# Performance work log

Hardware: AMD Instinct MI355X
Metric: run time of the kernel (lower is better)

Reference implementation:

```python
import jax, jax.numpy as jnp
import numpy as np

N = 4096       # nodes
E = 131072     # edges (avg degree 32)
IN_C = 512
HID = 512
OUT_C = 64
RANK = 64      # svd_q
N_DOM = 4
EPS = 1e-5     # BatchNorm eps


def setup_inputs() -> dict:
    key = jax.random.key(0)
    ks = jax.random.split(key, 12)
    x = jax.random.normal(ks[0], (N, IN_C), dtype=jnp.float32)
    row = jax.random.randint(ks[1], (E,), 0, N)
    off = jax.random.randint(ks[2], (E,), 1, N)
    col = (row + off) % N  # guarantee no pre-existing self loops
    edge_index = jnp.stack([row, col]).astype(jnp.int32)
    edge_weight = jax.random.uniform(ks[3], (E,), dtype=jnp.float32)
    y = jax.random.randint(ks[4], (N,), 0, N_DOM).astype(jnp.int32)
    W1 = jax.random.normal(ks[5], (IN_C, HID), dtype=jnp.float32) / np.sqrt(IN_C).astype(np.float32)
    b1 = jnp.zeros((HID,), jnp.float32)
    Wmu = jax.random.normal(ks[6], (HID, OUT_C), dtype=jnp.float32) / np.sqrt(HID).astype(np.float32)
    bmu = jnp.zeros((OUT_C,), jnp.float32)
    Wlv = jax.random.normal(ks[7], (HID, OUT_C), dtype=jnp.float32) / np.sqrt(HID).astype(np.float32)
    blv = jnp.zeros((OUT_C,), jnp.float32)
    gamma = jnp.ones((N_DOM, HID), jnp.float32)   # per-domain BN weight
    beta = jnp.zeros((N_DOM, HID), jnp.float32)   # per-domain BN bias
    return dict(x=x, edge_index=edge_index, edge_weight=edge_weight, y=y,
                W1=W1, b1=b1, Wmu=Wmu, bmu=bmu, Wlv=Wlv, blv=blv,
                gamma=gamma, beta=beta)


def _safe_rsqrt(deg):
    # PyG gcn_norm: deg^-0.5 with inf (and here non-positive) masked to 0
    safe = jnp.where(deg > 0, deg, 1.0)
    return jnp.where(deg > 0, 1.0 / jnp.sqrt(safe), 0.0)


def gcn_conv_edges(x, W, b, row, col, w, n):
    # GCNConv with edge weights: add remaining self loops (fill=1), symmetric norm
    loop = jnp.arange(n, dtype=row.dtype)
    row_f = jnp.concatenate([row, loop])
    col_f = jnp.concatenate([col, loop])
    w_f = jnp.concatenate([w, jnp.ones((n,), w.dtype)])
    deg = jax.ops.segment_sum(w_f, col_f, num_segments=n)
    dinv = _safe_rsqrt(deg)
    norm = dinv[row_f] * w_f * dinv[col_f]
    xw = x @ W                                   # [n, out]
    out = jax.ops.segment_sum(norm[:, None] * xw[row_f], col_f, num_segments=n)
    return out + b


def gcn_conv_dense(x, W, b, A):
    # Dense-adjacency GCNConv (reconstructed adjacency already has a diagonal,
    # so add_remaining_self_loops is a no-op). deg over target (col) index.
    deg = A.sum(axis=0)
    dinv = _safe_rsqrt(deg)
    Ahat = dinv[:, None] * A * dinv[None, :]     # [n, n] normalized
    return Ahat.T @ (x @ W) + b                  # aggregate at targets


def svd_lowrank_recon(A, q, niter=2):
    # torch.svd_lowrank-style randomized SVD, then U @ diag(s) @ V^T
    omega = jax.random.normal(jax.random.key(42), (A.shape[1], q), A.dtype)
    Qb = jnp.linalg.qr(A @ omega)[0]
    for _ in range(niter):
        Qb = jnp.linalg.qr(A.T @ Qb)[0]
        Qb = jnp.linalg.qr(A @ Qb)[0]
    B = Qb.T @ A                                 # [q, n]
    U, s, Vt = jnp.linalg.svd(B, full_matrices=False)
    return (Qb @ (U * s)) @ Vt                   # [n, n] low-rank reconstruction


def dsbn_relu(x, y, gamma, beta):
    # Domain-specific BatchNorm (training-mode batch stats per domain) + ReLU
    out = jnp.zeros_like(x)
    for i in range(N_DOM):
        m = (y == i)
        mf = m.astype(x.dtype)[:, None]
        cnt = jnp.maximum(mf.sum(), 1.0)
        mean = (x * mf).sum(0) / cnt
        var = (((x - mean) ** 2) * mf).sum(0) / cnt   # biased var, as BatchNorm
        xn = (x - mean) / jnp.sqrt(var + EPS) * gamma[i] + beta[i]
        out = jnp.where(m[:, None], xn, out)
    return jax.nn.relu(out)


def reference(x, edge_index, edge_weight, y, W1, b1, Wmu, bmu, Wlv, blv, gamma, beta):
    row, col = edge_index[0], edge_index[1]
    # ----- branch 1: original sparse graph -----
    h1 = dsbn_relu(gcn_conv_edges(x, W1, b1, row, col, edge_weight, N), y, gamma, beta)
    z_mean1 = gcn_conv_edges(h1, Wmu, bmu, row, col, edge_weight, N)
    z_log1 = gcn_conv_edges(h1, Wlv, blv, row, col, edge_weight, N)
    # ----- branch 2: SVD low-rank reconstructed (dense) graph -----
    A = jnp.zeros((N, N), x.dtype).at[row, col].add(edge_weight)  # coalesced COO
    A2 = svd_lowrank_recon(A, RANK)
    h2 = dsbn_relu(gcn_conv_dense(x, W1, b1, A2), y, gamma, beta)
    z_mean2 = gcn_conv_dense(h2, Wmu, bmu, A2)
    z_log2 = gcn_conv_dense(h2, Wlv, blv, A2)
    return (z_mean1, z_log1, z_mean2, z_log2)
```

## Files before the change

### kernel.cpp

```cpp
#include <hip/hip_runtime.h>
#include <hip/hip_bf16.h>


#define NN    4096
#define NEDG  131072
#define INC   512
#define HIDC  512
#define OUTC  64
#define RK    64
#define NDOM  4
#define EPSBN 1e-5f

typedef unsigned short ushortT;
typedef __attribute__((ext_vector_type(8))) short bf16x8;
typedef __attribute__((ext_vector_type(4))) float f32x4;

static inline int cdiv(int a, int b){ return (a + b - 1) / b; }

__device__ __forceinline__ float bf2f(unsigned u){ return __uint_as_float(u << 16); }

__global__ __launch_bounds__(256) void k_detect(const unsigned short* __restrict__ p,
                                                int* __restrict__ flag){
  int t = threadIdx.x;
  int cnt = 0;
  for (int i = t; i < 4096; i += 256){
    unsigned short v = p[2*i];
    int e = (v >> 7) & 0xFF;
    if (e >= 100 && e <= 140) cnt++;
  }
  __shared__ int sh[256];
  sh[t] = cnt; __syncthreads();
  for (int off = 128; off > 0; off >>= 1){ if (t < off) sh[t] += sh[t+off]; __syncthreads(); }
  if (t == 0) *flag = (sh[0] >= 2048) ? 0 : 1;
}

__device__ __forceinline__ float upc1(const void* s, int f, int off){
  return f ? ((const float*)s)[off]
           : __bfloat162float(((const __hip_bfloat16*)s)[off]);
}
__device__ __forceinline__ ushortT tobf(float v){
  __hip_bfloat16 h = __float2bfloat16(v);
  return *(ushortT*)&h;
}
#define SEG_X   2097152
#define SEG_W1  262144
#define SEG_W   131072
#define SEG_WMU 32768
#define SEG_GB  2048
#define SEG_B1  512
#define SEG_BO  64
#define OFF1 (SEG_X)
#define OFF2 (OFF1+SEG_W1)
#define OFF3 (OFF2+SEG_W)
#define OFF4 (OFF3+SEG_WMU)
#define OFF5 (OFF4+SEG_WMU)
#define OFF6 (OFF5+SEG_GB)
#define OFF7 (OFF6+SEG_GB)
#define OFF8 (OFF7+SEG_B1)
#define OFF9 (OFF8+SEG_BO)
#define OFFT (OFF9+SEG_BO)

__global__ __launch_bounds__(256) void k_upcast_all(
    const void* x, const void* W1, const void* w, const void* Wmu, const void* Wlv,
    const void* gm, const void* bt, const void* b1, const void* bmu, const void* blv,
    const int* __restrict__ isf32,
    float* dx, float* dW1, float* dw, float* dWmu, float* dWlv,
    float* dgm, float* dbt, float* db1, float* dbmu, float* dblv,
    ushortT* xbf, ushortT* W1bf, ushortT* Wmubf, ushortT* Wlvbf){
  int i = blockIdx.x*256 + threadIdx.x;
  if (i >= OFFT) return;
  int f = *isf32;
  if      (i < OFF1){ float v = upc1(x, f, i); dx[i] = v; xbf[i] = tobf(v); }
  else if (i < OFF2){ float v = upc1(W1, f, i - OFF1); dW1[i - OFF1] = v; W1bf[i - OFF1] = tobf(v); }
  else if (i < OFF3) dw  [i - OFF2] = upc1(w,   f, i - OFF2);
  else if (i < OFF4){ float v = upc1(Wmu, f, i - OFF3); dWmu[i - OFF3] = v; Wmubf[i - OFF3] = tobf(v); }
  else if (i < OFF5){ float v = upc1(Wlv, f, i - OFF4); dWlv[i - OFF4] = v; Wlvbf[i - OFF4] = tobf(v); }
  else if (i < OFF6) dgm [i - OFF5] = upc1(gm,  f, i - OFF5);
  else if (i < OFF7) dbt [i - OFF6] = upc1(bt,  f, i - OFF6);
  else if (i < OFF8) db1 [i - OFF7] = upc1(b1,  f, i - OFF7);
  else if (i < OFF9) dbmu[i - OFF8] = upc1(bmu, f, i - OFF8);
  else               dblv[i - OFF9] = upc1(blv, f, i - OFF9);
}

__global__ __launch_bounds__(256) void k_prep(float* deg, int* cntR, int* cntC, int* dcnt,
                                              float* bnsum){
  int i = blockIdx.x*256 + threadIdx.x;
  if (i < NN){ deg[i] = 1.0f; cntR[i] = 0; cntC[i] = 0; }
  if (i < NDOM) dcnt[i] = 0;
  if (i < 8*HIDC) bnsum[i] = 0.f;
}
__global__ __launch_bounds__(256) void k_fin(const double* __restrict__ Qd,
        float* __restrict__ Bf1, const double* __restrict__ Cd, float* __restrict__ Cm,
        const double* __restrict__ qs, float* __restrict__ dinv2,
        float* __restrict__ Tm, float* __restrict__ Um, float* __restrict__ bnsum){
  int i = blockIdx.x*256 + threadIdx.x;
  if (i < NN*RK){ Bf1[i] = (float)Qd[i]; Cm[i] = (float)Cd[i]; }
  if (i < NN){
    double s = 0.0;
    #pragma unroll
    for (int k = 0; k < RK; k++) s += Cd[(size_t)i*RK + k] * qs[k];
    dinv2[i] = (s > 0.0) ? (float)(1.0/sqrt(s)) : 0.f;
  }
  if (i < RK*HIDC) Tm[i] = 0.f;
  if (i < 2*RK*RK) Um[i] = 0.f;
  if (i < 8*HIDC)  bnsum[i] = 0.f;
}

__global__ __launch_bounds__(256) void k_hist(const int* __restrict__ row, const int* __restrict__ col,
                                              const float* __restrict__ w, float* deg,
                                              int* cntR, int* cntC){
  int e = blockIdx.x*256 + threadIdx.x;
  if (e < NEDG){
    atomicAdd(&deg[col[e]], w[e]);
    atomicAdd(&cntR[row[e]], 1);
    atomicAdd(&cntC[col[e]], 1);
  }
}
__global__ __launch_bounds__(256) void k_dinv(const float* deg, float* dinv, int n){
  int i = blockIdx.x*256 + threadIdx.x;
  if (i < n){ float d = deg[i]; dinv[i] = (d > 0.f) ? 1.f/sqrtf(d) : 0.f; }
}
__global__ __launch_bounds__(256) void k_norm1(const int* __restrict__ row, const int* __restrict__ col,
                                               const float* __restrict__ w, const float* __restrict__ dinv,
                                               float* __restrict__ nrm){
  int e = blockIdx.x*256 + threadIdx.x;
  if (e < NEDG) nrm[e] = dinv[row[e]] * w[e] * dinv[col[e]];
}
__global__ __launch_bounds__(1024) void k_scan4096(const int* __restrict__ cnt,
                                                   int* __restrict__ ptr, int* __restrict__ pos){
  __shared__ int sh[1024];
  int t = threadIdx.x;
  int b = t*4;
  int a0 = cnt[b], a1 = cnt[b+1], a2 = cnt[b+2], a3 = cnt[b+3];
  sh[t] = a0 + a1 + a2 + a3;
  __syncthreads();
  for (int off = 1; off < 1024; off <<= 1){
    int v = (t >= off) ? sh[t-off] : 0;
    __syncthreads();
    sh[t] += v;
    __syncthreads();
  }
  int excl = (t == 0) ? 0 : sh[t-1];
  ptr[b]   = excl;            pos[b]   = excl;
  ptr[b+1] = excl+a0;         pos[b+1] = excl+a0;
  ptr[b+2] = excl+a0+a1;      pos[b+2] = excl+a0+a1;
  ptr[b+3] = excl+a0+a1+a2;   pos[b+3] = excl+a0+a1+a2;
  if (t == 1023) ptr[4096] = sh[1023];
}
__global__ __launch_bounds__(256) void k_scatter(const int* __restrict__ row, const int* __restrict__ col,
                                                 int* posR, int* posC, int* eidR, int* eidC){
  int e = blockIdx.x*256 + threadIdx.x;
  if (e < NEDG){
    int p = atomicAdd(&posR[row[e]], 1); eidR[p] = e;
    int q = atomicAdd(&posC[col[e]], 1); eidC[q] = e;
  }
}
__global__ __launch_bounds__(256) void k_edges(const int* __restrict__ rowA, const int* __restrict__ colA,
        const float* __restrict__ wf, const float* __restrict__ nrm,
        const int* __restrict__ eidR, const int* __restrict__ eidC,
        int* __restrict__ csrSrc, float* __restrict__ csrW,
        int* __restrict__ cscSrc, float* __restrict__ cscW, float* __restrict__ cscN){
  int p = blockIdx.x*256 + threadIdx.x;
  if (p < NEDG){
    int eR = eidR[p]; csrSrc[p] = colA[eR]; csrW[p] = wf[eR];
    int eC = eidC[p]; cscSrc[p] = rowA[eC]; cscW[p] = wf[eC]; cscN[p] = nrm[eC];
  }
}
__global__ __launch_bounds__(256) void k_dcnt(const int* __restrict__ y, int* dcnt){
  int i = blockIdx.x*256 + threadIdx.x;
  if (i < NN) atomicAdd(&dcnt[y[i]], 1);
}

__device__ __forceinline__ unsigned rotl32(unsigned x, unsigned d){ return (x << d) | (x >> (32u - d)); }
#define TF_ROUND4(R0,R1,R2,R3) \
  x0 += x1; x1 = rotl32(x1,R0); x1 ^= x0; \
  x0 += x1; x1 = rotl32(x1,R1); x1 ^= x0; \
  x0 += x1; x1 = rotl32(x1,R2); x1 ^= x0; \
  x0 += x1; x1 = rotl32(x1,R3); x1 ^= x0;

__device__ __forceinline__ void tf2x32(unsigned k0, unsigned k1, unsigned c0, unsigned c1,
                                       unsigned* o0, unsigned* o1){
  unsigned ks2 = 0x1BD11BDAu ^ k0 ^ k1;
  unsigned x0 = c0 + k0, x1 = c1 + k1;
  TF_ROUND4(13,15,26,6);   x0 += k1;  x1 += ks2 + 1u;
  TF_ROUND4(17,29,16,24);  x0 += ks2; x1 += k0 + 2u;
  TF_ROUND4(13,15,26,6);   x0 += k0;  x1 += k1 + 3u;
  TF_ROUND4(17,29,16,24);  x0 += k1;  x1 += ks2 + 4u;
  TF_ROUND4(13,15,26,6);   x0 += ks2; x1 += k0 + 5u;
  *o0 = x0; *o1 = x1;
}

__device__ double erfinv64(double x){
  double w = -log1p(-x*x);
  double p;
  if (w < 5.0){
    w -= 2.5;
    p = 2.81022636e-08;  p = p*w + 3.43273939e-07; p = p*w - 3.5233877e-06;
    p = p*w - 4.39150654e-06; p = p*w + 0.00021858087; p = p*w - 0.00125372503;
    p = p*w - 0.00417768164;  p = p*w + 0.246640727;   p = p*w + 1.50140941;
  } else {
    w = sqrt(w) - 3.0;
    p = -0.000200214257; p = p*w + 0.000100950558; p = p*w + 0.00134934322;
    p = p*w - 0.00367342844; p = p*w + 0.00573950773; p = p*w - 0.0076224613;
    p = p*w + 0.00943887047; p = p*w + 1.00167406;    p = p*w + 2.83297682;
  }
  double y = p * x;
  const double c = 1.1283791670955126;
  #pragma unroll
  for (int it = 0; it < 3; it++){
    double err = erf(y) - x;
    y -= err / (c * exp(-y*y));
  }
  return y;
}

__device__ float bits_to_normal(unsigned b){
  float f = __uint_as_float((b >> 9) | 0x3f800000u) - 1.0f;
  const float lo = -0.99999994f;
  float x = fmaxf(lo, f * 2.0f + lo);
  double r = 1.4142135623730951 * erfinv64((double)x);
  return (float)r;
}

__global__ __launch_bounds__(256) void k_omega(float* __restrict__ om, double* __restrict__ Gd){
  int i = blockIdx.x*256 + threadIdx.x;
  if (i < RK*RK) Gd[i] = 0.0;
  if (i >= 262144) return;
  unsigned o0, o1;
  tf2x32(0u, 42u, 0u, (unsigned)i, &o0, &o1);
  om[i] = bits_to_normal(o0 ^ o1);
}

__global__ __launch_bounds__(256) void k_gemm_bf16(
    const ushortT* __restrict__ A, const ushortT* __restrict__ B,
    float* __restrict__ Cc, ushortT* __restrict__ Cbf){
  __shared__ ushortT As2[64][40];
  __shared__ ushortT Bs2[64][40];
  int t = threadIdx.x;
  int bm = blockIdx.y * 64, bn = blockIdx.x * 64;
  int w = t >> 6, l = t & 63;
  int lr = l & 15, lk = l >> 4;
  f32x4 acc[4] = {};
  int ar = t >> 2, ac = (t & 3) * 8;
  int bc = t & 63, bk = (t >> 6) * 8;
  for (int k0 = 0; k0 < 512; k0 += 32){
    *(uint4*)&As2[ar][ac] = *(const uint4*)&A[(size_t)(bm + ar) * 512 + k0 + ac];
    ushortT tmp[8];
    #pragma unroll
    for (int j = 0; j < 8; j++)
      tmp[j] = B[(size_t)(k0 + bk + j) * 512 + bn + bc];
    *(uint4*)&Bs2[bc][bk] = *(uint4*)tmp;
    __syncthreads();
    bf16x8 afrag = *(bf16x8*)&As2[w * 16 + lr][lk * 8];
    #pragma unroll
    for (int nt = 0; nt < 4; nt++){
      bf16x8 bfrag = *(bf16x8*)&Bs2[nt * 16 + lr][lk * 8];
      acc[nt] = __builtin_amdgcn_mfma_f32_16x16x32_bf16(afrag, bfrag, acc[nt], 0, 0, 0);
    }
    __syncthreads();
  }
  #pragma unroll
  for (int nt = 0; nt < 4; nt++){
    #pragma unroll
    for (int i = 0; i < 4; i++){
      size_t idx = (size_t)(bm + w * 16 + lk * 4 + i) * 512 + bn + nt * 16 + lr;
      float v = acc[nt][i];
      Cc[idx] = v;
      Cbf[idx] = tobf(v);
    }
  }
}

__device__ __forceinline__ void d_hw2(int bx, int t,
    const ushortT* __restrict__ A, const ushortT* __restrict__ Bm,
    const ushortT* __restrict__ Bl, float* __restrict__ Ca, float* __restrict__ Cb){
  __shared__ ushortT As2[64][40];
  __shared__ ushortT Bs2[64][40];
  int nb = NN/64;
  int second = bx >= nb;
  int bm = (bx - (second ? nb : 0)) * 64;
  const ushortT* B = second ? Bl : Bm;
  float* Cc = second ? Cb : Ca;
  int w = t >> 6, l = t & 63;
  int lr = l & 15, lk = l >> 4;
  f32x4 acc[4] = {};
  int ar = t >> 2, ac = (t & 3) * 8;
  int bc = t & 63, bk = (t >> 6) * 8;
  for (int k0 = 0; k0 < 512; k0 += 32){
    *(uint4*)&As2[ar][ac] = *(const uint4*)&A[(size_t)(bm + ar) * 512 + k0 + ac];
    ushortT tmp[8];
    #pragma unroll
    for (int j = 0; j < 8; j++)
      tmp[j] = B[(size_t)(k0 + bk + j) * 64 + bc];
    *(uint4*)&Bs2[bc][bk] = *(uint4*)tmp;
    __syncthreads();
    bf16x8 afrag = *(bf16x8*)&As2[w * 16 + lr][lk * 8];
    #pragma unroll
    for (int nt = 0; nt < 4; nt++){
      bf16x8 bfrag = *(bf16x8*)&Bs2[nt * 16 + lr][lk * 8];
      acc[nt] = __builtin_amdgcn_mfma_f32_16x16x32_bf16(afrag, bfrag, acc[nt], 0, 0, 0);
    }
    __syncthreads();
  }
  #pragma unroll
  for (int nt = 0; nt < 4; nt++){
    #pragma unroll
    for (int i = 0; i < 4; i++){
      Cc[(size_t)(bm + w * 16 + lk * 4 + i) * 64 + nt * 16 + lr] = acc[nt][i];
    }
  }
}
__global__ __launch_bounds__(256) void k_gemm_hw2(
    const ushortT* __restrict__ A, const ushortT* __restrict__ Bm,
    const ushortT* __restrict__ Bl, float* __restrict__ Ca, float* __restrict__ Cb){
  d_hw2(blockIdx.x, threadIdx.x, A, Bm, Bl, Ca, Cb);
}

__global__ __launch_bounds__(256) void k_gemm_nn(int M, int Nn, int K,
      const float* __restrict__ A, int lda, const float* __restrict__ B, int ldb,
      float* __restrict__ Cc, int ldc, const float* __restrict__ rowscale,
      const float* __restrict__ kscale, const float* __restrict__ bias){
  __shared__ float As[16][65];
  __shared__ float Bs[16][65];
  int bm = blockIdx.y*64, bn = blockIdx.x*64;
  int t = threadIdx.x;
  int tr = t >> 4, tc = t & 15;
  float acc[4][4] = {};
  for (int k0 = 0; k0 < K; k0 += 16){
    #pragma unroll
    for (int q = 0; q < 4; q++){
      int idx = t*4 + q;
      int m = idx >> 4, kk = idx & 15;
      As[kk][m] = A[(size_t)(bm+m)*lda + (k0+kk)];
    }
    #pragma unroll
    for (int q = 0; q < 4; q++){
      int idx = t + q*256;
      int kk = idx >> 6, n = idx & 63;
      float ks = kscale ? kscale[k0+kk] : 1.0f;
      Bs[kk][n] = B[(size_t)(k0+kk)*ldb + (bn+n)] * ks;
    }
    __syncthreads();
    #pragma unroll
    for (int kk = 0; kk < 16; kk++){
      float a0 = As[kk][tr*4+0], a1 = As[kk][tr*4+1], a2 = As[kk][tr*4+2], a3 = As[kk][tr*4+3];
      float b0 = Bs[kk][tc*4+0], b1 = Bs[kk][tc*4+1], b2 = Bs[kk][tc*4+2], b3 = Bs[kk][tc*4+3];
      acc[0][0] += a0*b0; acc[0][1] += a0*b1; acc[0][2] += a0*b2; acc[0][3] += a0*b3;
      acc[1][0] += a1*b0; acc[1][1] += a1*b1; acc[1][2] += a1*b2; acc[1][3] += a1*b3;
      acc[2][0] += a2*b0; acc[2][1] += a2*b1; acc[2][2] += a2*b2; acc[2][3] += a2*b3;
      acc[3][0] += a3*b0; acc[3][1] += a3*b1; acc[3][2] += a3*b2; acc[3][3] += a3*b3;
    }
    __syncthreads();
  }
  #pragma unroll
  for (int i2 = 0; i2 < 4; i2++){
    int m = bm + tr*4 + i2;
    float rs = rowscale ? rowscale[m] : 1.0f;
    #pragma unroll
    for (int j2 = 0; j2 < 4; j2++){
      int n = bn + tc*4 + j2;
      float v = acc[i2][j2] * rs;
      if (bias) v += bias[n];
      Cc[(size_t)m*ldc + n] = v;
    }
  }
}

__global__ __launch_bounds__(256) void k_gemm_nn2(
      const float* __restrict__ A, const float* __restrict__ Um,
      const float* __restrict__ rowscale,
      const float* __restrict__ bmu, const float* __restrict__ blv,
      float* __restrict__ zout){
  __shared__ float As[16][65];
  __shared__ float Bs[16][65];
  int z = blockIdx.z;
  const float* B = Um + (size_t)z*RK*RK;
  const float* bias = z ? blv : bmu;
  float* Cc = zout + (size_t)(2+z)*NN*OUTC;
  int bm = blockIdx.y*64;
  int t = threadIdx.x;
  int tr = t >> 4, tc = t & 15;
  float acc[4][4] = {};
  for (int k0 = 0; k0 < RK; k0 += 16){
    #pragma unroll
    for (int q = 0; q < 4; q++){
      int idx = t*4 + q;
      int m = idx >> 4, kk = idx & 15;
      As[kk][m] = A[(size_t)(bm+m)*RK + (k0+kk)];
    }
    #pragma unroll
    for (int q = 0; q < 4; q++){
      int idx = t + q*256;
      int kk = idx >> 6, n = idx & 63;
      Bs[kk][n] = B[(size_t)(k0+kk)*RK + n];
    }
    __syncthreads();
    #pragma unroll
    for (int kk = 0; kk < 16; kk++){
      float a0 = As[kk][tr*4+0], a1 = As[kk][tr*4+1], a2 = As[kk][tr*4+2], a3 = As[kk][tr*4+3];
      float b0 = Bs[kk][tc*4+0], b1 = Bs[kk][tc*4+1], b2 = Bs[kk][tc*4+2], b3 = Bs[kk][tc*4+3];
      acc[0][0] += a0*b0; acc[0][1] += a0*b1; acc[0][2] += a0*b2; acc[0][3] += a0*b3;
      acc[1][0] += a1*b0; acc[1][1] += a1*b1; acc[1][2] += a1*b2; acc[1][3] += a1*b3;
      acc[2][0] += a2*b0; acc[2][1] += a2*b1; acc[2][2] += a2*b2; acc[2][3] += a2*b3;
      acc[3][0] += a3*b0; acc[3][1] += a3*b1; acc[3][2] += a3*b2; acc[3][3] += a3*b3;
    }
    __syncthreads();
  }
  #pragma unroll
  for (int i2 = 0; i2 < 4; i2++){
    int m = bm + tr*4 + i2;
    float rs = rowscale[m];
    #pragma unroll
    for (int j2 = 0; j2 < 4; j2++){
      int n = tc*4 + j2;
      Cc[(size_t)m*OUTC + n] = acc[i2][j2] * rs + bias[n];
    }
  }
}

__global__ __launch_bounds__(256) void k_gemm_tn_sk(int M, int Nn, int K, int kchunk,
      const float* __restrict__ A, int lda, const float* __restrict__ B, int ldb,
      float* __restrict__ Cc, int ldc, const float* __restrict__ kscale){
  __shared__ float As[32][17];
  __shared__ float Bs[32][17];
  int bm = blockIdx.y*16, bn = blockIdx.x*16;
  int kb = blockIdx.z*kchunk, ke = kb + kchunk;
  int t = threadIdx.x;
  int tm = t >> 4, tn = t & 15;
  float acc = 0.f;
  for (int k0 = kb; k0 < ke; k0 += 32){
    #pragma unroll
    for (int q = 0; q < 2; q++){
      int idx = t + q*256;
      int kk = idx >> 4, m = idx & 15;
      float sv = kscale ? kscale[k0+kk] : 1.0f;
      As[kk][m] = A[(size_t)(k0+kk)*lda + (bm+m)] * sv;
      Bs[kk][m] = B[(size_t)(k0+kk)*ldb + (bn+m)];
    }
    __syncthreads();
    #pragma unroll
    for (int kk = 0; kk < 32; kk++) acc += As[kk][tm] * Bs[kk][tn];
    __syncthreads();
  }
  atomicAdd(&Cc[(size_t)(bm+tm)*ldc + (bn+tn)], acc);
}

__global__ __launch_bounds__(256) void k_gemm_tn_sk2(
      const float* __restrict__ A,
      const float* __restrict__ Ba, const float* __restrict__ Bb,
      float* __restrict__ Um, const float* __restrict__ kscale){
  __shared__ float As[32][17];
  __shared__ float Bs[32][17];
  int z = blockIdx.z;
  int second = z >= 16;
  int kb = (second ? z - 16 : z) * 256, ke = kb + 256;
  const float* B = second ? Bb : Ba;
  float* Cc = Um + (second ? RK*RK : 0);
  int bm = blockIdx.y*16, bn = blockIdx.x*16;
  int t = threadIdx.x;
  int tm = t >> 4, tn = t & 15;
  float acc = 0.f;
  for (int k0 = kb; k0 < ke; k0 += 32){
    #pragma unroll
    for (int q = 0; q < 2; q++){
      int idx = t + q*256;
      int kk = idx >> 4, m = idx & 15;
      As[kk][m] = A[(size_t)(k0+kk)*RK + (bm+m)] * kscale[k0+kk];
      Bs[kk][m] = B[(size_t)(k0+kk)*OUTC + (bn+m)];
    }
    __syncthreads();
    #pragma unroll
    for (int kk = 0; kk < 32; kk++) acc += As[kk][tm] * Bs[kk][tn];
    __syncthreads();
  }
  atomicAdd(&Cc[(size_t)(bm+tm)*RK + (bn+tn)], acc);
}

__global__ __launch_bounds__(64) void k_spmm32(const int* __restrict__ ptr,
                       const int* __restrict__ src, const float* __restrict__ cf,
                       const float* __restrict__ X, float* __restrict__ Y){
  int seg = blockIdx.x;
  int t = threadIdx.x;
  double acc = 0.0;
  int p0 = ptr[seg], p1 = ptr[seg+1];
  for (int p = p0; p < p1; ++p){
    acc += (double)cf[p] * (double)X[(size_t)src[p]*RK + t];
  }
  Y[(size_t)seg*RK + t] = (float)acc;
}
__global__ __launch_bounds__(64) void k_spmm32to64(const int* __restrict__ ptr,
                       const int* __restrict__ src, const float* __restrict__ cf,
                       const float* __restrict__ X, double* __restrict__ Y){
  int seg = blockIdx.x;
  int t = threadIdx.x;
  double acc = 0.0;
  int p0 = ptr[seg], p1 = ptr[seg+1];
  for (int p = p0; p < p1; ++p){
    acc += (double)cf[p] * (double)X[(size_t)src[p]*RK + t];
  }
  Y[(size_t)seg*RK + t] = acc;
}
__global__ __launch_bounds__(256) void k_gram64(const double* __restrict__ X, double* __restrict__ G){
  __shared__ double Xs[64][65];
  int b = blockIdx.x;
  int t = threadIdx.x;
  #pragma unroll
  for (int q = 0; q < 16; q++){
    int idx = t + q*256;
    Xs[idx >> 6][idx & 63] = X[(size_t)(b*64 + (idx >> 6))*RK + (idx & 63)];
  }
  __syncthreads();
  int i = t >> 2;
  int j0 = (t & 3) * 16;
  double acc[16];
  #pragma unroll
  for (int jj = 0; jj < 16; jj++) acc[jj] = 0.0;
  for (int k = 0; k < 64; k++){
    double a = Xs[k][i];
    #pragma unroll
    for (int jj = 0; jj < 16; jj++) acc[jj] += a * Xs[k][j0+jj];
  }
  #pragma unroll
  for (int jj = 0; jj < 16; jj++) atomicAdd(&G[i*RK + j0 + jj], acc[jj]);
}

#define CHOLF_CHUNK(I0) \
  for (int k2 = 0; k2 < 16; k2++){ \
    int k = (I0) + k2; \
    int buf = k & 1; \
    if (t < 64 && j == k){ \
      double d = sqrt(fmax(cdiag, 1e-300)); \
      double s = 1.0 / d; \
      myd = d; \
      sdd[k] = s; \
      _Pragma("unroll") \
      for (int i = (I0); i < 64; i++){ c[i] *= s; colk[buf][i] = c[i]; } \
    } \
    __syncthreads(); \
    if (t < 64 && j > k && j < 64){ \
      double cj = colk[buf][j]; \
      cdiag -= cj * cj; \
      _Pragma("unroll") \
      for (int i = (I0); i < 64; i++){ c[i] -= colk[buf][i] * cj; } \
    } \
    __syncthreads(); \
  }

__global__ __launch_bounds__(256) void k_chol_spmm(
    double* __restrict__ G, double* __restrict__ sdd,
    const int* __restrict__ ptr, const int* __restrict__ src, const float* __restrict__ cf,
    const ushortT* __restrict__ Xb, float* __restrict__ Y,
    const float* __restrict__ self_dinv, const float* __restrict__ bias){
  __shared__ double colk[2][64];
  int t = threadIdx.x;
  if (blockIdx.x == 0){
    int j = t;
    double c[64];
    double cdiag = 0.0, myd = 0.0;
    if (t < 64){
      #pragma unroll
      for (int i = 0; i < 64; i++) c[i] = G[i*64 + j];
      #pragma unroll
      for (int i = 0; i < 64; i++) if (i == j) cdiag = c[i];
    }
    CHOLF_CHUNK(0)
    CHOLF_CHUNK(16)
    CHOLF_CHUNK(32)
    CHOLF_CHUNK(48)
    if (t < 64){
      #pragma unroll
      for (int i = 0; i < 64; i++){
        double v = (i > j) ? c[i] : 0.0;
        if (i == j) v = myd;
        G[i*64 + j] = v;
      }
    }
  } else {
    int seg = blockIdx.x - 1;
    float acc0, acc1;
    {
      float sd = self_dinv[seg]; float s2 = sd*sd;
      unsigned v = *(const unsigned*)&Xb[(size_t)seg*HIDC + 2*t];
      acc0 = s2 * bf2f(v & 0xffffu);
      acc1 = s2 * bf2f(v >> 16);
    }
    int p0 = ptr[seg], p1 = ptr[seg+1];
    for (int p = p0; p < p1; ++p){
      int o = src[p];
      float cc = cf[p];
      unsigned v = *(const unsigned*)&Xb[(size_t)o*HIDC + 2*t];
      acc0 += cc * bf2f(v & 0xffffu);
      acc1 += cc * bf2f(v >> 16);
    }
    acc0 += bias[2*t];
    acc1 += bias[2*t+1];
    Y[(size_t)seg*HIDC + 2*t]     = acc0;
    Y[(size_t)seg*HIDC + 2*t + 1] = acc1;
  }
}

__device__ __forceinline__ void d_bnpart(int b, int t,
    const float* __restrict__ H, const int* __restrict__ y, float* __restrict__ bnsum){
  int j0 = 2*t;
  float s00=0,s01=0,s10=0,s11=0,s20=0,s21=0,s30=0,s31=0;
  float q00=0,q01=0,q10=0,q11=0,q20=0,q21=0,q30=0,q31=0;
  int r0 = b*32;
  for (int r = r0; r < r0+32; r++){
    int d = y[r];
    float2 v = *(const float2*)&H[(size_t)r*HIDC + j0];
    float ax = v.x, ay = v.y;
    float bx = ax*ax, by = ay*ay;
    if      (d == 0){ s00+=ax; s01+=ay; q00+=bx; q01+=by; }
    else if (d == 1){ s10+=ax; s11+=ay; q10+=bx; q11+=by; }
    else if (d == 2){ s20+=ax; s21+=ay; q20+=bx; q21+=by; }
    else            { s30+=ax; s31+=ay; q30+=bx; q31+=by; }
  }
  atomicAdd(&bnsum[0*HIDC+j0], s00); atomicAdd(&bnsum[0*HIDC+j0+1], s01);
  atomicAdd(&bnsum[1*HIDC+j0], s10); atomicAdd(&bnsum[1*HIDC+j0+1], s11);
  atomicAdd(&bnsum[2*HIDC+j0], s20); atomicAdd(&bnsum[2*HIDC+j0+1], s21);
  atomicAdd(&bnsum[3*HIDC+j0], s30); atomicAdd(&bnsum[3*HIDC+j0+1], s31);
  atomicAdd(&bnsum[4*HIDC+j0], q00); atomicAdd(&bnsum[4*HIDC+j0+1], q01);
  atomicAdd(&bnsum[5*HIDC+j0], q10); atomicAdd(&bnsum[5*HIDC+j0+1], q11);
  atomicAdd(&bnsum[6*HIDC+j0], q20); atomicAdd(&bnsum[6*HIDC+j0+1], q21);
  atomicAdd(&bnsum[7*HIDC+j0], q30); atomicAdd(&bnsum[7*HIDC+j0+1], q31);
}
__global__ __launch_bounds__(256) void k_bnpart(const float* __restrict__ H,
        const int* __restrict__ y, float* __restrict__ bnsum){
  d_bnpart(blockIdx.x, threadIdx.x, H, y, bnsum);
}

__device__ __forceinline__ void d_bnapply(int idx,
    float* __restrict__ H, const int* __restrict__ y,
    const float* __restrict__ bnsum, const int* __restrict__ dcnt,
    const float* __restrict__ gamma, const float* __restrict__ beta,
    ushortT* __restrict__ Hbf){
  int n = idx >> 9, j = idx & (HIDC-1);
  int d = y[n];
  float cnt  = fmaxf((float)dcnt[d], 1.0f);
  float mean = bnsum[d*HIDC + j] / cnt;
  float var  = fmaxf(bnsum[(4+d)*HIDC + j] / cnt - mean*mean, 0.f);
  float inv  = 1.0f / sqrtf(var + EPSBN);
  float gmm  = gamma[d*HIDC + j];
  float scal = gmm * inv;
  float shft = beta[d*HIDC + j] - mean * gmm * inv;
  float v = H[idx] * scal + shft;
  v = v > 0.f ? v : 0.f;
  H[idx] = v;
  Hbf[idx] = tobf(v);
}
__global__ __launch_bounds__(256) void k_bnapply(float* __restrict__ H, const int* __restrict__ y,
        const float* __restrict__ bnsum, const int* __restrict__ dcnt,
        const float* __restrict__ gamma, const float* __restrict__ beta,
        ushortT* __restrict__ Hbf){
  int idx = blockIdx.x*256 + threadIdx.x;
  if (idx < NN*HIDC) d_bnapply(idx, H, y, bnsum, dcnt, gamma, beta, Hbf);
}

__global__ __launch_bounds__(256) void k_trinv_bn(const double* __restrict__ L,
      const double* __restrict__ sdd, double* __restrict__ Rinv,
      const float* __restrict__ H, const int* __restrict__ y, float* __restrict__ bnsum){
  int t = threadIdx.x;
  if (blockIdx.x > 0){
    d_bnpart(blockIdx.x - 1, t, H, y, bnsum);
    return;
  }
  __shared__ double gl[64][65];
  __shared__ double Xl[64][65];
  __shared__ double sdinv[64];
  __shared__ double Sl[3][16][17];
  #pragma unroll
  for (int q = 0; q < 16; q++){
    int idx = t + (q << 8);
    gl[idx >> 6][idx & 63] = L[idx];
  }
  if (t < 64) sdinv[t] = sdd[t];
  for (int idx = t; idx < 64*65; idx += 256)
    ((double*)Xl)[idx] = 0.0;
  __syncthreads();
  if (t < 64){
    int b = t >> 4, c2 = t & 15;
    int g0 = b << 4;
    int gc = g0 + c2;
    Xl[gc][gc] = sdinv[gc];
    for (int i = c2 - 1; i >= 0; i--){
      int gi = g0 + i;
      double s = 0.0;
      for (int k2 = i + 1; k2 <= c2; k2++)
        s += gl[g0 + k2][gi] * Xl[g0 + k2][gc];
      Xl[gi][gc] = -s * sdinv[gi];
    }
  }
  __syncthreads();
  for (int d = 1; d < 4; d++){
    int np = 4 - d;
    int tot = np << 8;
    for (int e = t; e < tot; e += 256){
      int p = e >> 8;
      int i = (e >> 4) & 15, jj = e & 15;
      int gi = (p << 4) + i, gj = ((p + d) << 4) + jj;
      double s = 0.0;
      int a0 = (p + 1) << 4, a1 = (p + d + 1) << 4;
      for (int a = a0; a < a1; a++)
        s += gl[a][gi] * Xl[a][gj];
      Sl[p][i][jj] = s;
    }
    __syncthreads();
    for (int e = t; e < tot; e += 256){
      int p = e >> 8;
      int i = (e >> 4) & 15, jj = e & 15;
      int gi = (p << 4) + i, gj = ((p + d) << 4) + jj;
      double s = 0.0;
      #pragma unroll
      for (int k2 = 0; k2 < 16; k2++)
        s += Xl[gi][(p << 4) + k2] * Sl[p][k2][jj];
      Xl[gi][gj] = -s;
    }
    __syncthreads();
  }
  #pragma unroll
  for (int q = 0; q < 16; q++){
    int e2 = t + (q << 8);
    Rinv[e2] = Xl[e2 >> 6][e2 & 63];
  }
}

__global__ __launch_bounds__(256) void k_applyR_bn(const double* __restrict__ srcQ,
      const double* __restrict__ Rinv, double* __restrict__ dst,
      float* __restrict__ H, const int* __restrict__ y,
      const float* __restrict__ bnsum, const int* __restrict__ dcnt,
      const float* __restrict__ gamma, const float* __restrict__ beta,
      ushortT* __restrict__ Hbf){
  int t = threadIdx.x;
  if (blockIdx.x >= NN/4){
    int idx = (blockIdx.x - NN/4)*256 + t;
    if (idx < NN*HIDC) d_bnapply(idx, H, y, bnsum, dcnt, gamma, beta, Hbf);
    return;
  }
  __shared__ double Rs[64][65];
  #pragma unroll
  for (int q = 0; q < 16; q++){
    int idx = t + q*256;
    Rs[idx >> 6][idx & 63] = Rinv[idx];
  }
  __syncthreads();
  int r = blockIdx.x*4 + (t >> 6);
  int j = t & 63;
  const double* rowp = srcQ + (size_t)r*RK;
  double s = 0.0;
  for (int k = 0; k <= j; k++) s += rowp[k] * Rs[k][j];
  dst[(size_t)r*RK + j] = s;
}

__global__ __launch_bounds__(256) void k_spmmC_hw2(
    const int* __restrict__ ptr, const int* __restrict__ src, const float* __restrict__ cf,
    const double* __restrict__ X, double* __restrict__ Y,
    const ushortT* __restrict__ A, const ushortT* __restrict__ Bm,
    const ushortT* __restrict__ Bl, float* __restrict__ Ca, float* __restrict__ Cb){
  int t = threadIdx.x;
  if (blockIdx.x >= NN/4){
    d_hw2(blockIdx.x - NN/4, t, A, Bm, Bl, Ca, Cb);
    return;
  }
  int seg = blockIdx.x*4 + (t >> 6);
  int lane = t & 63;
  double acc = 0.0;
  int p0 = ptr[seg], p1 = ptr[seg+1];
  for (int p = p0; p < p1; ++p){
    acc += (double)cf[p] * X[(size_t)src[p]*RK + lane];
  }
  Y[(size_t)seg*RK + lane] = acc;
}

__global__ __launch_bounds__(256) void k_qsum_spmm2(
    const double* __restrict__ Q, double* __restrict__ qs,
    const int* __restrict__ ptr, const int* __restrict__ src, const float* __restrict__ cf,
    const float* __restrict__ Xa, const float* __restrict__ Xb2,
    float* __restrict__ zout, const float* __restrict__ self_dinv,
    const float* __restrict__ bmu, const float* __restrict__ blv){
  int t = threadIdx.x;
  if (blockIdx.x < 64){
    int j = blockIdx.x;
    double a = 0.0;
    for (int n = t; n < NN; n += 256) a += Q[(size_t)n*RK + j];
    __shared__ double sh[256];
    sh[t] = a; __syncthreads();
    for (int off = 128; off > 0; off >>= 1){ if (t < off) sh[t] += sh[t+off]; __syncthreads(); }
    if (t == 0) qs[j] = sh[0];
    return;
  }
  int bb = blockIdx.x - 64;
  int second = bb >= NN/4;
  int seg = (second ? bb - NN/4 : bb)*4 + (t >> 6);
  int lane = t & 63;
  const float* X = second ? Xb2 : Xa;
  const float* bias = second ? blv : bmu;
  float* Y = zout + (second ? (size_t)NN*OUTC : 0);
  float acc0;
  {
    float sd = self_dinv[seg];
    acc0 = sd*sd * X[(size_t)seg*OUTC + lane];
  }
  int p0 = ptr[seg], p1 = ptr[seg+1];
  for (int p = p0; p < p1; ++p){
    acc0 += cf[p] * X[(size_t)src[p]*OUTC + lane];
  }
  acc0 += bias[lane];
  Y[(size_t)seg*OUTC + lane] = acc0;
}

extern "C" void kernel_launch(void* const* d_in, const int* in_sizes, int n_in,
                              void* d_out, int out_size, void* d_ws, size_t ws_size,
                              hipStream_t stream){
  (void)in_sizes; (void)n_in; (void)out_size;
  const void* x_in  = d_in[0];
  const int*  ei    = (const int*)d_in[1];
  const void* w_in  = d_in[2];
  const int*  yv    = (const int*)d_in[3];
  const void* W1i   = d_in[4];
  const void* b1i   = d_in[5];
  const void* Wmui  = d_in[6];
  const void* bmui  = d_in[7];
  const void* Wlvi  = d_in[8];
  const void* blvi  = d_in[9];
  const void* gmi   = d_in[10];
  const void* bti   = d_in[11];
  const int* rowA = ei;
  const int* colA = ei + NEDG;
  float* zout = (float*)d_out;

  double* Dp = (double*)d_ws;
  size_t od = 0;
  double* Qd0 = Dp + od; od += (size_t)NN*RK;
  double* Qd1 = Dp + od; od += (size_t)NN*RK;
  double* Cd  = Dp + od; od += (size_t)NN*RK;
  double* Gd  = Dp + od; od += RK*RK;
  double* Rid = Dp + od; od += RK*RK;
  double* qsd = Dp + od; od += RK;
  double* sdd = Dp + od; od += RK;
  float* Fp = (float*)(Dp + od);
  size_t o = 0;
  float* xf   = Fp + o; o += (size_t)NN*INC;
  float* W1f  = Fp + o; o += (size_t)INC*HIDC;
  float* b1f  = Fp + o; o += HIDC;
  float* Wmuf = Fp + o; o += (size_t)HIDC*OUTC;
  float* bmuf = Fp + o; o += OUTC;
  float* Wlvf = Fp + o; o += (size_t)HIDC*OUTC;
  float* blvf = Fp + o; o += OUTC;
  float* gmf  = Fp + o; o += NDOM*HIDC;
  float* btf  = Fp + o; o += NDOM*HIDC;
  float* wf   = Fp + o; o += NEDG;
  float* xw1  = Fp + o; o += (size_t)NN*HIDC;
  float* hwA  = Fp + o; o += (size_t)NN*OUTC;
  float* hwB  = Fp + o; o += (size_t)NN*OUTC;
  float* Bf1  = Fp + o; o += (size_t)NN*RK;
  float* Cm   = Fp + o; o += (size_t)NN*RK;
  float* Qf0  = Fp + o; o += (size_t)NN*RK;
  float* Qf1  = Fp + o; o += (size_t)NN*RK;
  float* Tm   = Fp + o; o += (size_t)RK*HIDC;
  float* Umu  = Fp + o; o += 2*RK*RK;
  float* deg1 = Fp + o; o += NN;
  float* dinv1= Fp + o; o += NN;
  float* dinv2= Fp + o; o += NN;
  float* norm1= Fp + o; o += NEDG;
  float* bnsum= Fp + o; o += 8*HIDC;
  float* csrW = Fp + o; o += NEDG;
  float* cscW = Fp + o; o += NEDG;
  float* cscN = Fp + o; o += NEDG;
  ushortT* xbf   = (ushortT*)(Fp + o); o += (size_t)NN*INC/2;
  ushortT* W1bf  = (ushortT*)(Fp + o); o += (size_t)INC*HIDC/2;
  ushortT* xw1bf = (ushortT*)(Fp + o); o += (size_t)NN*HIDC/2;
  ushortT* hbf   = (ushortT*)(Fp + o); o += (size_t)NN*HIDC/2;
  ushortT* Wmubf = (ushortT*)(Fp + o); o += (size_t)HIDC*OUTC/2;
  ushortT* Wlvbf = (ushortT*)(Fp + o); o += (size_t)HIDC*OUTC/2;
  int* Ip = (int*)(Fp + o);
  size_t oi = 0;
  int* cntR = Ip + oi; oi += NN;
  int* ptrR = Ip + oi; oi += NN + 1;
  int* posR = Ip + oi; oi += NN;
  int* eidR = Ip + oi; oi += NEDG;
  int* cntC = Ip + oi; oi += NN;
  int* ptrC = Ip + oi; oi += NN + 1;
  int* posC = Ip + oi; oi += NN;
  int* eidC = Ip + oi; oi += NEDG;
  int* csrSrc = Ip + oi; oi += NEDG;
  int* cscSrc = Ip + oi; oi += NEDG;
  int* dcnt = Ip + oi; oi += NDOM;
  int* dflag= Ip + oi; oi += 1;

  size_t need = od*sizeof(double) + o*sizeof(float) + (oi+16)*sizeof(int);
  if (ws_size < need) return;

  float* hbuf = xf;

  const int T = 256;
  k_detect<<<1,T,0,stream>>>((const unsigned short*)x_in, dflag);
  k_upcast_all<<<cdiv(OFFT,T),T,0,stream>>>(
      x_in, W1i, w_in, Wmui, Wlvi, gmi, bti, b1i, bmui, blvi, dflag,
      xf, W1f, wf, Wmuf, Wlvf, gmf, btf, b1f, bmuf, blvf,
      xbf, W1bf, Wmubf, Wlvbf);

  k_prep<<<cdiv(NN,T),T,0,stream>>>(deg1, cntR, cntC, dcnt, bnsum);
  k_hist <<<cdiv(NEDG,T),T,0,stream>>>(rowA, colA, wf, deg1, cntR, cntC);
  k_dinv <<<cdiv(NN,T),T,0,stream>>>(deg1, dinv1, NN);
  k_norm1<<<cdiv(NEDG,T),T,0,stream>>>(rowA, colA, wf, dinv1, norm1);
  k_scan4096<<<1,1024,0,stream>>>(cntR, ptrR, posR);
  k_scan4096<<<1,1024,0,stream>>>(cntC, ptrC, posC);
  k_scatter<<<cdiv(NEDG,T),T,0,stream>>>(rowA, colA, posR, posC, eidR, eidC);
  k_edges<<<cdiv(NEDG,T),T,0,stream>>>(rowA, colA, wf, norm1, eidR, eidC,
                                       csrSrc, csrW, cscSrc, cscW, cscN);
  k_omega<<<cdiv(NN*RK,T),T,0,stream>>>(Qf0, Gd);
  k_dcnt <<<cdiv(NN,T),T,0,stream>>>(yv, dcnt);

  k_gemm_bf16<<<dim3(HIDC/64, NN/64),256,0,stream>>>(xbf, W1bf, xw1, xw1bf);

  k_spmm32<<<NN,64,0,stream>>>(ptrR, csrSrc, csrW, Qf0, Qf1);
  k_spmm32<<<NN,64,0,stream>>>(ptrC, cscSrc, cscW, Qf1, Qf0);
  k_spmm32<<<NN,64,0,stream>>>(ptrR, csrSrc, csrW, Qf0, Qf1);
  k_spmm32<<<NN,64,0,stream>>>(ptrC, cscSrc, cscW, Qf1, Qf0);
  k_spmm32to64<<<NN,64,0,stream>>>(ptrR, csrSrc, csrW, Qf0, Qd1);
  k_gram64<<<NN/64,256,0,stream>>>(Qd1, Gd);

  k_chol_spmm<<<NN+1,256,0,stream>>>(Gd, sdd, ptrC, cscSrc, cscN, xw1bf, hbuf,
                                     dinv1, b1f);
  k_trinv_bn<<<1+NN/32,256,0,stream>>>(Gd, sdd, Rid, hbuf, yv, bnsum);
  k_applyR_bn<<<NN/4 + cdiv(NN*HIDC,T),256,0,stream>>>(Qd1, Rid, Qd0,
      hbuf, yv, bnsum, dcnt, gmf, btf, hbf);
  k_spmmC_hw2<<<NN/4 + 2*(NN/64),256,0,stream>>>(ptrC, cscSrc, cscW, Qd0, Cd,
      hbf, Wmubf, Wlvbf, hwA, hwB);
  k_qsum_spmm2<<<64 + 2*(NN/4),256,0,stream>>>(Qd0, qsd, ptrC, cscSrc, cscN,
      hwA, hwB, zout, dinv1, bmuf, blvf);
  k_fin<<<cdiv(NN*RK,T),T,0,stream>>>(Qd0, Bf1, Cd, Cm, qsd, dinv2, Tm, Umu, bnsum);

  k_gemm_tn_sk<<<dim3(HIDC/16, RK/16, 8),256,0,stream>>>(RK,HIDC,NN,512, Bf1,RK, xw1,HIDC, Tm,HIDC, dinv2);
  k_gemm_nn<<<dim3(HIDC/64, NN/64),256,0,stream>>>(NN,HIDC,RK, Cm,RK, Tm,HIDC, hbuf,HIDC, dinv2, nullptr, b1f);
  k_bnpart<<<NN/32,256,0,stream>>>(hbuf, yv, bnsum);
  k_bnapply<<<cdiv(NN*HIDC,T),T,0,stream>>>(hbuf, yv, bnsum, dcnt, gmf, btf, hbf);
  k_gemm_hw2<<<2*(NN/64),256,0,stream>>>(hbf, Wmubf, Wlvbf, hwA, hwB);
  k_gemm_tn_sk2<<<dim3(RK/16, RK/16, 32),256,0,stream>>>(Bf1, hwA, hwB, Umu, dinv2);
  k_gemm_nn2<<<dim3(1, NN/64, 2),256,0,stream>>>(Cm, Umu, dinv2, bmuf, blvf, zout);
}
```

Baseline: 556.3 us.

## Fuse finalize into spmm kernels, pack four segments per block, use fp32 C

The separate k_fin launch is removed. The Q fp32 copy is now written inside k_applyR_bn, the column-sum reduction and the C sparse product are fused with the hw2 GEMM, and the dinv2/zeroing work is folded into the second spmm kernel. This cuts three launches down to two and drops the double-precision C buffer. The small spmm kernels now process four segments per 256-thread block instead of one per 64-thread block. C is now built from fp32 Q rather than double Q, which slightly changes accumulation precision.

```diff
diff --git a/kernel.cpp b/kernel.cpp
--- a/kernel.cpp
+++ b/kernel.cpp
@@ -89,22 +89,6 @@
   if (i < NDOM) dcnt[i] = 0;
   if (i < 8*HIDC) bnsum[i] = 0.f;
 }
-__global__ __launch_bounds__(256) void k_fin(const double* __restrict__ Qd,
-        float* __restrict__ Bf1, const double* __restrict__ Cd, float* __restrict__ Cm,
-        const double* __restrict__ qs, float* __restrict__ dinv2,
-        float* __restrict__ Tm, float* __restrict__ Um, float* __restrict__ bnsum){
-  int i = blockIdx.x*256 + threadIdx.x;
-  if (i < NN*RK){ Bf1[i] = (float)Qd[i]; Cm[i] = (float)Cd[i]; }
-  if (i < NN){
-    double s = 0.0;
-    #pragma unroll
-    for (int k = 0; k < RK; k++) s += Cd[(size_t)i*RK + k] * qs[k];
-    dinv2[i] = (s > 0.0) ? (float)(1.0/sqrt(s)) : 0.f;
-  }
-  if (i < RK*HIDC) Tm[i] = 0.f;
-  if (i < 2*RK*RK) Um[i] = 0.f;
-  if (i < 8*HIDC)  bnsum[i] = 0.f;
-}
 
 __global__ __launch_bounds__(256) void k_hist(const int* __restrict__ row, const int* __restrict__ col,
                                               const float* __restrict__ w, float* deg,
@@ -476,29 +460,29 @@
   atomicAdd(&Cc[(size_t)(bm+tm)*RK + (bn+tn)], acc);
 }
 
-__global__ __launch_bounds__(64) void k_spmm32(const int* __restrict__ ptr,
+__global__ __launch_bounds__(256) void k_spmm32x4(const int* __restrict__ ptr,
                        const int* __restrict__ src, const float* __restrict__ cf,
                        const float* __restrict__ X, float* __restrict__ Y){
-  int seg = blockIdx.x;
-  int t = threadIdx.x;
+  int seg = blockIdx.x*4 + (threadIdx.x >> 6);
+  int lane = threadIdx.x & 63;
   double acc = 0.0;
   int p0 = ptr[seg], p1 = ptr[seg+1];
   for (int p = p0; p < p1; ++p){
-    acc += (double)cf[p] * (double)X[(size_t)src[p]*RK + t];
-  }
-  Y[(size_t)seg*RK + t] = (float)acc;
-}
-__global__ __launch_bounds__(64) void k_spmm32to64(const int* __restrict__ ptr,
+    acc += (double)cf[p] * (double)X[(size_t)src[p]*RK + lane];
+  }
+  Y[(size_t)seg*RK + lane] = (float)acc;
+}
+__global__ __launch_bounds__(256) void k_spmm32to64x4(const int* __restrict__ ptr,
                        const int* __restrict__ src, const float* __restrict__ cf,
                        const float* __restrict__ X, double* __restrict__ Y){
-  int seg = blockIdx.x;
-  int t = threadIdx.x;
+  int seg = blockIdx.x*4 + (threadIdx.x >> 6);
+  int lane = threadIdx.x & 63;
   double acc = 0.0;
   int p0 = ptr[seg], p1 = ptr[seg+1];
   for (int p = p0; p < p1; ++p){
-    acc += (double)cf[p] * (double)X[(size_t)src[p]*RK + t];
-  }
-  Y[(size_t)seg*RK + t] = acc;
+    acc += (double)cf[p] * (double)X[(size_t)src[p]*RK + lane];
+  }
+  Y[(size_t)seg*RK + lane] = acc;
 }
 __global__ __launch_bounds__(256) void k_gram64(const double* __restrict__ X, double* __restrict__ G){
   __shared__ double Xs[64][65];
@@ -725,7 +709,7 @@
 }
 
 __global__ __launch_bounds__(256) void k_applyR_bn(const double* __restrict__ srcQ,
-      const double* __restrict__ Rinv, double* __restrict__ dst,
+      const double* __restrict__ Rinv, double* __restrict__ dst, float* __restrict__ Bf1,
       float* __restrict__ H, const int* __restrict__ y,
       const float* __restrict__ bnsum, const int* __restrict__ dcnt,
       const float* __restrict__ gamma, const float* __restrict__ beta,
@@ -749,34 +733,15 @@
   double s = 0.0;
   for (int k = 0; k <= j; k++) s += rowp[k] * Rs[k][j];
   dst[(size_t)r*RK + j] = s;
-}
-
-__global__ __launch_bounds__(256) void k_spmmC_hw2(
+  Bf1[(size_t)r*RK + j] = (float)s;
+}
+
+__global__ __launch_bounds__(256) void k_qsum_spmmC_hw2(
+    const double* __restrict__ Q, double* __restrict__ qs,
     const int* __restrict__ ptr, const int* __restrict__ src, const float* __restrict__ cf,
-    const double* __restrict__ X, double* __restrict__ Y,
+    const float* __restrict__ Xf, float* __restrict__ Cm,
     const ushortT* __restrict__ A, const ushortT* __restrict__ Bm,
     const ushortT* __restrict__ Bl, float* __restrict__ Ca, float* __restrict__ Cb){
-  int t = threadIdx.x;
-  if (blockIdx.x >= NN/4){
-    d_hw2(blockIdx.x - NN/4, t, A, Bm, Bl, Ca, Cb);
-    return;
-  }
-  int seg = blockIdx.x*4 + (t >> 6);
-  int lane = t & 63;
-  double acc = 0.0;
-  int p0 = ptr[seg], p1 = ptr[seg+1];
-  for (int p = p0; p < p1; ++p){
-    acc += (double)cf[p] * X[(size_t)src[p]*RK + lane];
-  }
-  Y[(size_t)seg*RK + lane] = acc;
-}
-
-__global__ __launch_bounds__(256) void k_qsum_spmm2(
-    const double* __restrict__ Q, double* __restrict__ qs,
-    const int* __restrict__ ptr, const int* __restrict__ src, const float* __restrict__ cf,
-    const float* __restrict__ Xa, const float* __restrict__ Xb2,
-    float* __restrict__ zout, const float* __restrict__ self_dinv,
-    const float* __restrict__ bmu, const float* __restrict__ blv){
   int t = threadIdx.x;
   if (blockIdx.x < 64){
     int j = blockIdx.x;
@@ -788,7 +753,42 @@
     if (t == 0) qs[j] = sh[0];
     return;
   }
-  int bb = blockIdx.x - 64;
+  if (blockIdx.x < 64 + NN/4){
+    int seg = (blockIdx.x - 64)*4 + (t >> 6);
+    int lane = t & 63;
+    double acc = 0.0;
+    int p0 = ptr[seg], p1 = ptr[seg+1];
+    for (int p = p0; p < p1; ++p){
+      acc += (double)cf[p] * (double)Xf[(size_t)src[p]*RK + lane];
+    }
+    Cm[(size_t)seg*RK + lane] = (float)acc;
+    return;
+  }
+  d_hw2(blockIdx.x - 64 - NN/4, t, A, Bm, Bl, Ca, Cb);
+}
+
+__global__ void k_fin_spmm2(
+    const float* __restrict__ Cm, const double* __restrict__ qs, float* __restrict__ dinv2,
+    float* __restrict__ Tm, float* __restrict__ Um, float* __restrict__ bnsum,
+    const int* __restrict__ ptr, const int* __restrict__ src, const float* __restrict__ cf,
+    const float* __restrict__ Xa, const float* __restrict__ Xb2,
+    float* __restrict__ zout, const float* __restrict__ self_dinv,
+    const float* __restrict__ bmu, const float* __restrict__ blv){
+  int t = threadIdx.x;
+  if (blockIdx.x < 128){
+    int idx = blockIdx.x*256 + t;
+    Tm[idx] = 0.f;
+    if (idx < 2*RK*RK) Um[idx] = 0.f;
+    if (idx < 8*HIDC)  bnsum[idx] = 0.f;
+    if (idx < NN){
+      double s = 0.0;
+      #pragma unroll
+      for (int k = 0; k < RK; k++) s += (double)Cm[(size_t)idx*RK + k] * qs[k];
+      dinv2[idx] = (s > 0.0) ? (float)(1.0/sqrt(s)) : 0.f;
+    }
+    return;
+  }
+  int bb = blockIdx.x - 128;
   int second = bb >= NN/4;
   int seg = (second ? bb - NN/4 : bb)*4 + (t >> 6);
   int lane = t & 63;
@@ -832,7 +832,6 @@
   size_t od = 0;
   double* Qd0 = Dp + od; od += (size_t)NN*RK;
   double* Qd1 = Dp + od; od += (size_t)NN*RK;
-  double* Cd  = Dp + od; od += (size_t)NN*RK;
   double* Gd  = Dp + od; od += RK*RK;
   double* Rid = Dp + od; od += RK*RK;
   double* qsd = Dp + od; od += RK;
@@ -913,23 +912,22 @@
 
   k_gemm_bf16<<<dim3(HIDC/64, NN/64),256,0,stream>>>(xbf, W1bf, xw1, xw1bf);
 
-  k_spmm32<<<NN,64,0,stream>>>(ptrR, csrSrc, csrW, Qf0, Qf1);
-  k_spmm32<<<NN,64,0,stream>>>(ptrC, cscSrc, cscW, Qf1, Qf0);
-  k_spmm32<<<NN,64,0,stream>>>(ptrR, csrSrc, csrW, Qf0, Qf1);
-  k_spmm32<<<NN,64,0,stream>>>(ptrC, cscSrc, cscW, Qf1, Qf0);
-  k_spmm32to64<<<NN,64,0,stream>>>(ptrR, csrSrc, csrW, Qf0, Qd1);
+  k_spmm32x4<<<NN/4,256,0,stream>>>(ptrR, csrSrc, csrW, Qf0, Qf1);
+  k_spmm32x4<<<NN/4,256,0,stream>>>(ptrC, cscSrc, cscW, Qf1, Qf0);
+  k_spmm32x4<<<NN/4,256,0,stream>>>(ptrR, csrSrc, csrW, Qf0, Qf1);
+  k_spmm32x4<<<NN/4,256,0,stream>>>(ptrC, cscSrc, cscW, Qf1, Qf0);
+  k_spmm32to64x4<<<NN/4,256,0,stream>>>(ptrR, csrSrc, csrW, Qf0, Qd1);
   k_gram64<<<NN/64,256,0,stream>>>(Qd1, Gd);
 
   k_chol_spmm<<<NN+1,256,0,stream>>>(Gd, sdd, ptrC, cscSrc, cscN, xw1bf, hbuf,
                                      dinv1, b1f);
   k_trinv_bn<<<1+NN/32,256,0,stream>>>(Gd, sdd, Rid, hbuf, yv, bnsum);
-  k_applyR_bn<<<NN/4 + cdiv(NN*HIDC,T),256,0,stream>>>(Qd1, Rid, Qd0,
+  k_applyR_bn<<<NN/4 + cdiv(NN*HIDC,T),256,0,stream>>>(Qd1, Rid, Qd0, Bf1,
       hbuf, yv, bnsum, dcnt, gmf, btf, hbf);
-  k_spmmC_hw2<<<NN/4 + 2*(NN/64),256,0,stream>>>(ptrC, cscSrc, cscW, Qd0, Cd,
-      hbf, Wmubf, Wlvbf, hwA, hwB);
-  k_qsum_spmm2<<<64 + 2*(NN/4),256,0,stream>>>(Qd0, qsd, ptrC, cscSrc, cscN,
-      hwA, hwB, zout, dinv1, bmuf, blvf);
-  k_fin<<<cdiv(NN*RK,T),T,0,stream>>>(Qd0, Bf1, Cd, Cm, qsd, dinv2, Tm, Umu, bnsum);
+  k_qsum_spmmC_hw2<<<64 + NN/4 + 2*(NN/64),256,0,stream>>>(Qd0, qsd,
+      ptrC, cscSrc, cscW, Bf1, Cm, hbf, Wmubf, Wlvbf, hwA, hwB);
+  k_fin_spmm2<<<128 + 2*(NN/4),256,0,stream>>>(Cm, qsd, dinv2, Tm, Umu, bnsum,
+      ptrC, cscSrc, cscN, hwA, hwB, zout, dinv1, bmuf, blvf);
 
   k_gemm_tn_sk<<<dim3(HIDC/16, RK/16, 8),256,0,stream>>>(RK,HIDC,NN,512, Bf1,RK, xw1,HIDC, Tm,HIDC, dinv2);
   k_gemm_nn<<<dim3(HIDC/64, NN/64),256,0,stream>>>(NN,HIDC,RK, Cm,RK, Tm,HIDC, hbuf,HIDC, dinv2, nullptr, b1f);
```

New measurement: 574.4 us. +3.2%, slower.
